# Kernel tuning notes

Hardware: AMD Instinct MI355X
Metric: run time of the kernel (lower is better)

## Reference

```python
import jax, jax.numpy as jnp
import numpy as np

N_NODES = 100000
N_EDGES = 1600000
IN_DIM = 128
HID = 64
HEADS = 8
OUTF = HID // HEADS  # out_feats per head = 8
ATTN_SLOPE = 0.2     # DGL GATConv leaky_relu slope for attention logits
ACT_SLOPE = 0.01     # F.leaky_relu default slope for inter-layer activation


def leaky_relu(x, slope):
    return jnp.where(x >= 0, x, slope * x)


def gat_layer(x, src, dst, W, al, ar, b, apply_act):
    # x: [N, Din], W: [Din, H*F], al/ar: [H, F], b: [H*F]
    N = x.shape[0]
    feat = (x @ W).reshape(N, HEADS, OUTF)                     # [N, H, F]
    el = jnp.sum(feat * al[None], axis=-1)                      # [N, H]
    er = jnp.sum(feat * ar[None], axis=-1)                      # [N, H]
    e = leaky_relu(el[src] + er[dst], ATTN_SLOPE)               # [E, H]
    # segment softmax over incoming edges of each dst node
    m = jax.ops.segment_max(e, dst, num_segments=N)             # [N, H]
    ex = jnp.exp(e - m[dst])                                    # [E, H]
    s = jax.ops.segment_sum(ex, dst, num_segments=N)            # [N, H]
    alpha = ex / s[dst]                                         # [E, H]
    msg = feat[src] * alpha[:, :, None]                         # [E, H, F]
    rst = jax.ops.segment_sum(msg, dst, num_segments=N)         # [N, H, F]
    rst = rst + b.reshape(1, HEADS, OUTF)
    if apply_act:
        rst = leaky_relu(rst, ACT_SLOPE)
    return rst.reshape(N, HEADS * OUTF)


def setup_inputs() -> dict:
    key = jax.random.key(0)
    ks = jax.random.split(key, 12)
    n_feat = jax.random.normal(ks[0], (N_NODES, IN_DIM), dtype=jnp.float32)
    src = jax.random.randint(ks[1], (N_EDGES,), 0, N_NODES, dtype=jnp.int32)
    dst = jax.random.randint(ks[2], (N_EDGES,), 0, N_NODES, dtype=jnp.int32)
    sc = 0.1
    W0 = sc * jax.random.normal(ks[3], (IN_DIM, HID), dtype=jnp.float32)
    al0 = sc * jax.random.normal(ks[4], (HEADS, OUTF), dtype=jnp.float32)
    ar0 = sc * jax.random.normal(ks[5], (HEADS, OUTF), dtype=jnp.float32)
    b0 = jnp.zeros((HID,), dtype=jnp.float32)
    W1 = sc * jax.random.normal(ks[6], (HID, HID), dtype=jnp.float32)
    al1 = sc * jax.random.normal(ks[7], (HEADS, OUTF), dtype=jnp.float32)
    ar1 = sc * jax.random.normal(ks[8], (HEADS, OUTF), dtype=jnp.float32)
    b1 = jnp.zeros((HID,), dtype=jnp.float32)
    return {"n_feat": n_feat, "src": src, "dst": dst,
            "W0": W0, "al0": al0, "ar0": ar0, "b0": b0,
            "W1": W1, "al1": al1, "ar1": ar1, "b1": b1}


def reference(n_feat, src, dst, W0, al0, ar0, b0, W1, al1, ar1, b1):
    h = gat_layer(n_feat, src, dst, W0, al0, ar0, b0, apply_act=True)
    h = gat_layer(h, src, dst, W1, al1, ar1, b1, apply_act=False)
    return h
```

## Files before the change

### kernel.cpp

```cpp
#include <hip/hip_runtime.h>
#include <math.h>

#define NN 100000
#define NE 1600000
#define ATTN_SLOPE 0.2f
#define ACT_SLOPE 0.01f

#define NBUK 512
#define BK 196
#define NBLK 1024
#define CHUNK ((NE + NBLK - 1) / NBLK)
#define CAP 5120

typedef __attribute__((ext_vector_type(8))) short bf16x8;
typedef __attribute__((ext_vector_type(4))) float f32x4;

__global__ void __launch_bounds__(256) count_kernel(const int* __restrict__ dst,
                                                    int* __restrict__ counts) {
    __shared__ int h[NBUK];
    const int blk = blockIdx.x;
    for (int i = threadIdx.x; i < NBUK; i += 256) h[i] = 0;
    __syncthreads();
    const int beg = blk * CHUNK;
    const int end = (beg + CHUNK < NE) ? beg + CHUNK : NE;
    for (int i = beg + threadIdx.x; i < end; i += 256)
        atomicAdd(&h[dst[i] / BK], 1);
    __syncthreads();
    for (int i = threadIdx.x; i < NBUK; i += 256)
        counts[blk * NBUK + i] = h[i];
}

__global__ void __launch_bounds__(NBLK) scanA(const int* __restrict__ counts,
                                              int* __restrict__ wbase, int* __restrict__ btot) {
    __shared__ int lds[NBLK];
    const int b = blockIdx.x;
    const int t = threadIdx.x;
    const int v = counts[t * NBUK + b];
    lds[t] = v;
    __syncthreads();
    for (int off = 1; off < NBLK; off <<= 1) {
        int u = (t >= off) ? lds[t - off] : 0;
        __syncthreads();
        lds[t] += u;
        __syncthreads();
    }
    wbase[t * NBUK + b] = lds[t] - v;
    if (t == NBLK - 1) btot[b] = lds[t];
}

__global__ void __launch_bounds__(NBUK) scan_bucket(const int* __restrict__ btot,
                                                    int* __restrict__ bbase, int* __restrict__ offs) {
    __shared__ int lds[NBUK];
    const int t = threadIdx.x;
    const int v = btot[t];
    lds[t] = v;
    __syncthreads();
    for (int off = 1; off < NBUK; off <<= 1) {
        int u = (t >= off) ? lds[t - off] : 0;
        __syncthreads();
        lds[t] += u;
        __syncthreads();
    }
    bbase[t] = lds[t] - v;
    if (t == NBUK - 1) { bbase[NBUK] = lds[t]; offs[NN] = lds[t]; }
}

__global__ void __launch_bounds__(256) scatter_radix(const int* __restrict__ src,
                                                     const int* __restrict__ dst,
                                                     const int* __restrict__ wbase,
                                                     const int* __restrict__ bbase,
                                                     int* __restrict__ tmp) {
    __shared__ int base[NBUK];
    __shared__ int cur[NBUK];
    const int blk = blockIdx.x;
    for (int i = threadIdx.x; i < NBUK; i += 256) {
        base[i] = bbase[i] + wbase[blk * NBUK + i];
        cur[i] = 0;
    }
    __syncthreads();
    const int beg = blk * CHUNK;
    const int end = (beg + CHUNK < NE) ? beg + CHUNK : NE;
    for (int i = beg + threadIdx.x; i < end; i += 256) {
        const int d = dst[i];
        const int b = d / BK;
        const int r = atomicAdd(&cur[b], 1);
        tmp[base[b] + r] = (src[i] << 8) | (d - b * BK);
    }
}

__global__ void __launch_bounds__(256) bucket_build(const int* __restrict__ tmp,
                                                    const int* __restrict__ bbase,
                                                    int* __restrict__ offs,
                                                    int* __restrict__ csr_src) {
    __shared__ int epack[CAP];
    __shared__ int csr_loc[CAP];
    __shared__ int cnt[256];
    __shared__ int loff[256];
    const int b = blockIdx.x;
    const int t = threadIdx.x;
    const int ebeg = bbase[b];
    const int nE = bbase[b + 1] - ebeg;
    const int nlo = b * BK;
    const int nn = (nlo < NN) ? ((NN - nlo < BK) ? (NN - nlo) : BK) : 0;
    const bool fits = (nE <= CAP);

    cnt[t] = 0;
    __syncthreads();
    for (int i = t; i < nE; i += 256) {
        const int p = tmp[ebeg + i];
        if (fits) epack[i] = p;
        atomicAdd(&cnt[p & 255], 1);
    }
    __syncthreads();
    const int v = cnt[t];
    for (int off = 1; off < 256; off <<= 1) {
        int u = (t >= off) ? cnt[t - off] : 0;
        __syncthreads();
        cnt[t] += u;
        __syncthreads();
    }
    const int excl = cnt[t] - v;
    loff[t] = excl;
    __syncthreads();
    cnt[t] = 0;
    if (t < nn) offs[nlo + t] = ebeg + excl;
    __syncthreads();
    for (int i = t; i < nE; i += 256) {
        const int p = fits ? epack[i] : tmp[ebeg + i];
        const int dloc = p & 255;
        const int pos = loff[dloc] + atomicAdd(&cnt[dloc], 1);
        if (fits) csr_loc[pos] = p >> 8;
        else csr_src[ebeg + pos] = p >> 8;
    }
    __syncthreads();
    if (fits)
        for (int i = t; i < nE; i += 256) csr_src[ebeg + i] = csr_loc[i];
}

__device__ __forceinline__ unsigned short bfr(float f) {
    unsigned int u = __builtin_bit_cast(unsigned int, f);
    return (unsigned short)((u + 0x7fffu + ((u >> 16) & 1u)) >> 16);
}
__device__ __forceinline__ float bf2f(unsigned short h) {
    return __builtin_bit_cast(float, ((unsigned int)h) << 16);
}
__device__ __forceinline__ float leaky_attn(float e) {
    return fmaf(0.4f, fabsf(e), 0.6f * e);
}

template <int DIN>
__global__ void __launch_bounds__(256) gemm_mfma_kernel(
        const float* __restrict__ x, const float* __restrict__ W,
        const float* __restrict__ al, const float* __restrict__ ar,
        unsigned short* __restrict__ feat, float* __restrict__ el, float* __restrict__ er,
        int nPairTiles) {
    constexpr int KS = DIN / 32;
    const int lane = threadIdx.x & 63;
    const int tw = threadIdx.x >> 6;
    const int colhalf = tw & 1;
    const int l15 = lane & 15;
    const int g = lane >> 4;
    const int colbase = colhalf * 32;

    bf16x8 Bhi[KS][2], Blo[KS][2];
#pragma unroll
    for (int ks = 0; ks < KS; ++ks) {
#pragma unroll
        for (int ct = 0; ct < 2; ++ct) {
            const int col = colbase + ct * 16 + l15;
#pragma unroll
            for (int j = 0; j < 8; ++j) {
                float w = W[(ks * 32 + g * 8 + j) * 64 + col];
                unsigned short h = bfr(w);
                Bhi[ks][ct][j] = (short)h;
                Blo[ks][ct][j] = (short)bfr(w - bf2f(h));
            }
        }
    }
    const float alc0 = al[colbase + l15];
    const float arc0 = ar[colbase + l15];
    const float alc1 = al[colbase + 16 + l15];
    const float arc1 = ar[colbase + 16 + l15];

#pragma unroll 1
    for (int pt = blockIdx.x; pt < nPairTiles; pt += gridDim.x) {
        const int rb = pt * 32 + (tw >> 1) * 16;
        f32x4 acc0 = {0.f, 0.f, 0.f, 0.f};
        f32x4 acc1 = {0.f, 0.f, 0.f, 0.f};
#pragma unroll
        for (int ks = 0; ks < KS; ++ks) {
            const float* xp = x + (size_t)(rb + l15) * DIN + ks * 32 + g * 8;
            f32x4 xa = *(const f32x4*)xp;
            f32x4 xb = *(const f32x4*)(xp + 4);
            bf16x8 Ahi, Alo;
#pragma unroll
            for (int j = 0; j < 4; ++j) {
                unsigned short h = bfr(xa[j]);
                Ahi[j] = (short)h;
                Alo[j] = (short)bfr(xa[j] - bf2f(h));
            }
#pragma unroll
            for (int j = 0; j < 4; ++j) {
                unsigned short h = bfr(xb[j]);
                Ahi[4 + j] = (short)h;
                Alo[4 + j] = (short)bfr(xb[j] - bf2f(h));
            }
            acc0 = __builtin_amdgcn_mfma_f32_16x16x32_bf16(Ahi, Bhi[ks][0], acc0, 0, 0, 0);
            acc0 = __builtin_amdgcn_mfma_f32_16x16x32_bf16(Ahi, Blo[ks][0], acc0, 0, 0, 0);
            acc0 = __builtin_amdgcn_mfma_f32_16x16x32_bf16(Alo, Bhi[ks][0], acc0, 0, 0, 0);
            acc1 = __builtin_amdgcn_mfma_f32_16x16x32_bf16(Ahi, Bhi[ks][1], acc1, 0, 0, 0);
            acc1 = __builtin_amdgcn_mfma_f32_16x16x32_bf16(Ahi, Blo[ks][1], acc1, 0, 0, 0);
            acc1 = __builtin_amdgcn_mfma_f32_16x16x32_bf16(Alo, Bhi[ks][1], acc1, 0, 0, 0);
        }
#pragma unroll
        for (int i = 0; i < 4; ++i) {
            const int n = rb + g * 4 + i;
            feat[(size_t)n * 64 + colbase + l15] = bfr(acc0[i]);
            feat[(size_t)n * 64 + colbase + 16 + l15] = bfr(acc1[i]);
            float vl0 = acc0[i] * alc0, vr0 = acc0[i] * arc0;
            float vl1 = acc1[i] * alc1, vr1 = acc1[i] * arc1;
#pragma unroll
            for (int d = 1; d < 8; d <<= 1) {
                vl0 += __shfl_xor(vl0, d); vr0 += __shfl_xor(vr0, d);
                vl1 += __shfl_xor(vl1, d); vr1 += __shfl_xor(vr1, d);
            }
            if ((lane & 7) == 0) {
                const int hb = (l15 >> 3) & 1;
                const int h0 = colbase / 8;
                el[n * 8 + h0 + hb] = vl0;
                er[n * 8 + h0 + hb] = vr0;
                el[n * 8 + h0 + 2 + hb] = vl1;
                er[n * 8 + h0 + 2 + hb] = vr1;
            }
        }
    }
}

__global__ void __launch_bounds__(128) aggregate_kernel(
        const unsigned short* __restrict__ feat, const float* __restrict__ el,
        const float* __restrict__ er,
        const int* __restrict__ csr_src, const int* __restrict__ offs,
        const float* __restrict__ bias, float* __restrict__ out, int N, int apply_act) {
    const int lane = threadIdx.x & 63;
    int node = (blockIdx.x << 1) + (threadIdx.x >> 6);
    if (node >= N) return;
    node = __builtin_amdgcn_readfirstlane(node);
    const int h = lane >> 3;
    const int beg = __builtin_amdgcn_readfirstlane(offs[node]);
    const int end = __builtin_amdgcn_readfirstlane(offs[node + 1]);
    const float er_n = er[node * 8 + h];

    float s0a = 0.f, s1a = 0.f, a0a = 0.f, a1a = 0.f;

    if (beg < end) {
        int si[8];
#pragma unroll
        for (int j = 0; j < 8; ++j) {
            const int idx = beg + j;
            si[j] = csr_src[idx < end ? idx : end - 1];
        }
#pragma unroll 1
        for (int k = beg; k < end; k += 8) {
            const int kn = k + 8;
            int sn[8];
            if (kn < end) {
#pragma unroll
                for (int j = 0; j < 8; ++j) {
                    const int idx = kn + j;
                    sn[j] = csr_src[idx < end ? idx : end - 1];
                }
            }
            unsigned short fu[8];
            float ev[8];
#pragma unroll
            for (int j = 0; j < 8; ++j) fu[j] = feat[(unsigned)(si[j] * 64 + lane)];
#pragma unroll
            for (int j = 0; j < 8; ++j) ev[j] = el[(unsigned)(si[j] * 8 + h)] + er_n;
#pragma unroll
            for (int j = 0; j < 8; ++j) {
                float p = __expf(leaky_attn(ev[j]));
                p = (k + j < end) ? p : 0.f;
                if (j & 1) { s1a += p; a1a = fmaf(p, bf2f(fu[j]), a1a); }
                else       { s0a += p; a0a = fmaf(p, bf2f(fu[j]), a0a); }
            }
            if (kn < end) {
#pragma unroll
                for (int j = 0; j < 8; ++j) si[j] = sn[j];
            }
        }
    }

    const float s = s0a + s1a;
    const float acc = a0a + a1a;
    float r = (s > 0.f) ? (acc / s) : 0.f;
    r += bias[lane];
    if (apply_act) r = (r >= 0.f) ? r : ACT_SLOPE * r;
    out[(size_t)node * 64 + lane] = r;
}

extern "C" void kernel_launch(void* const* d_in, const int* in_sizes, int n_in,
                              void* d_out, int out_size, void* d_ws, size_t ws_size,
                              hipStream_t stream) {
    const float* n_feat = (const float*)d_in[0];
    const int*   src    = (const int*)d_in[1];
    const int*   dst    = (const int*)d_in[2];
    const float* W0     = (const float*)d_in[3];
    const float* al0    = (const float*)d_in[4];
    const float* ar0    = (const float*)d_in[5];
    const float* b0     = (const float*)d_in[6];
    const float* W1     = (const float*)d_in[7];
    const float* al1    = (const float*)d_in[8];
    const float* ar1    = (const float*)d_in[9];
    const float* b1     = (const float*)d_in[10];
    float* out = (float*)d_out;

    char* ws = (char*)d_ws;
    size_t off = 0;
    auto alloc = [&](size_t bytes) -> void* {
        void* p = ws + off;
        off += (bytes + 255) & ~(size_t)255;
        return p;
    };
    unsigned short* featA = (unsigned short*)alloc((size_t)NN * 64 * 2);
    float* featB   = (float*)alloc((size_t)NN * 64 * 4);
    float* el      = (float*)alloc((size_t)NN * 8 * 4);
    float* er      = (float*)alloc((size_t)NN * 8 * 4);
    int*   offs    = (int*)alloc((size_t)(NN + 1) * 4);
    int*   csr_src = (int*)alloc((size_t)NE * 4);
    int*   tmp     = (int*)alloc((size_t)NE * 4);
    int*   counts  = (int*)alloc((size_t)NBLK * NBUK * 4);
    int*   wbase   = (int*)alloc((size_t)NBLK * NBUK * 4);
    int*   btot    = (int*)alloc((size_t)NBUK * 4);
    int*   bbase   = (int*)alloc((size_t)(NBUK + 1) * 4);

    count_kernel<<<NBLK, 256, 0, stream>>>(dst, counts);
    scanA<<<NBUK, NBLK, 0, stream>>>(counts, wbase, btot);
    scan_bucket<<<1, NBUK, 0, stream>>>(btot, bbase, offs);
    scatter_radix<<<NBLK, 256, 0, stream>>>(src, dst, wbase, bbase, tmp);
    bucket_build<<<NBUK, 256, 0, stream>>>(tmp, bbase, offs, csr_src);

    const int nPairTiles = NN / 32;

    gemm_mfma_kernel<128><<<nPairTiles, 256, 0, stream>>>(n_feat, W0, al0, ar0, featA, el, er, nPairTiles);
    aggregate_kernel<<<(NN + 1) / 2, 128, 0, stream>>>(featA, el, er, csr_src, offs, b0, featB, NN, 1);

    gemm_mfma_kernel<64><<<nPairTiles, 256, 0, stream>>>(featB, W1, al1, ar1, featA, el, er, nPairTiles);
    aggregate_kernel<<<(NN + 1) / 2, 128, 0, stream>>>(featA, el, er, csr_src, offs, b1, out, NN, 0);
}
```

Measured before the change: 211.7 us.

## Split wavefront into two half-waves processing alternate edges with packed bf16 loads

The aggregate kernel now lets each 32-lane half of the wavefront handle a different incoming edge, with each lane loading two packed bf16 features as one 32-bit word instead of one 16-bit value. The two halves are combined with a cross-half shuffle before one half writes a float2. This halves the exp and attention-logit work per lane and widens each memory access. In exchange it drops the software prefetch of the next batch of source indices and adds a tail loop plus a shuffle reduction.

```diff
diff --git a/kernel.cpp b/kernel.cpp
--- a/kernel.cpp
+++ b/kernel.cpp
@@ -245,57 +245,61 @@
     int node = (blockIdx.x << 1) + (threadIdx.x >> 6);
     if (node >= N) return;
     node = __builtin_amdgcn_readfirstlane(node);
-    const int h = lane >> 3;
+    const int e2 = lane >> 5;
+    const int l32 = lane & 31;
+    const int h = l32 >> 2;
     const int beg = __builtin_amdgcn_readfirstlane(offs[node]);
     const int end = __builtin_amdgcn_readfirstlane(offs[node + 1]);
     const float er_n = er[node * 8 + h];
 
-    float s0a = 0.f, s1a = 0.f, a0a = 0.f, a1a = 0.f;
-
-    if (beg < end) {
+    float s = 0.f, ax = 0.f, ay = 0.f;
+    int k = beg;
+    for (; k + 8 <= end; k += 8) {
         int si[8];
 #pragma unroll
-        for (int j = 0; j < 8; ++j) {
-            const int idx = beg + j;
-            si[j] = csr_src[idx < end ? idx : end - 1];
-        }
-#pragma unroll 1
-        for (int k = beg; k < end; k += 8) {
-            const int kn = k + 8;
-            int sn[8];
-            if (kn < end) {
-#pragma unroll
-                for (int j = 0; j < 8; ++j) {
-                    const int idx = kn + j;
-                    sn[j] = csr_src[idx < end ? idx : end - 1];
-                }
-            }
-            unsigned short fu[8];
-            float ev[8];
-#pragma unroll
-            for (int j = 0; j < 8; ++j) fu[j] = feat[(unsigned)(si[j] * 64 + lane)];
-#pragma unroll
-            for (int j = 0; j < 8; ++j) ev[j] = el[(unsigned)(si[j] * 8 + h)] + er_n;
-#pragma unroll
-            for (int j = 0; j < 8; ++j) {
-                float p = __expf(leaky_attn(ev[j]));
-                p = (k + j < end) ? p : 0.f;
-                if (j & 1) { s1a += p; a1a = fmaf(p, bf2f(fu[j]), a1a); }
-                else       { s0a += p; a0a = fmaf(p, bf2f(fu[j]), a0a); }
-            }
-            if (kn < end) {
-#pragma unroll
-                for (int j = 0; j < 8; ++j) si[j] = sn[j];
-            }
-        }
-    }
-
-    const float s = s0a + s1a;
-    const float acc = a0a + a1a;
-    float r = (s > 0.f) ? (acc / s) : 0.f;
-    r += bias[lane];
-    if (apply_act) r = (r >= 0.f) ? r : ACT_SLOPE * r;
-    out[(size_t)node * 64 + lane] = r;
+        for (int j = 0; j < 8; ++j) si[j] = csr_src[k + j];
+        unsigned fv[4];
+        float ev[4];
+#pragma unroll
+        for (int pp = 0; pp < 4; ++pp) {
+            const int sj = si[2 * pp + e2];
+            fv[pp] = *(const unsigned*)(feat + ((unsigned)sj * 64 + l32 * 2));
+            ev[pp] = el[(unsigned)(sj * 8 + h)] + er_n;
+        }
+#pragma unroll
+        for (int pp = 0; pp < 4; ++pp) {
+            const float p = __expf(leaky_attn(ev[pp]));
+            s += p;
+            ax = fmaf(p, bf2f((unsigned short)(fv[pp] & 0xffff)), ax);
+            ay = fmaf(p, bf2f((unsigned short)(fv[pp] >> 16)), ay);
+        }
+    }
+    for (; k < end; k += 2) {
+        const int idx = k + e2;
+        const int sj = csr_src[idx < end ? idx : end - 1];
+        const unsigned fv = *(const unsigned*)(feat + ((unsigned)sj * 64 + l32 * 2));
+        float p = __expf(leaky_attn(el[(unsigned)(sj * 8 + h)] + er_n));
+        p = (idx < end) ? p : 0.f;
+        s += p;
+        ax = fmaf(p, bf2f((unsigned short)(fv & 0xffff)), ax);
+        ay = fmaf(p, bf2f((unsigned short)(fv >> 16)), ay);
+    }
+
+    s  += __shfl_xor(s, 32, 64);
+    ax += __shfl_xor(ax, 32, 64);
+    ay += __shfl_xor(ay, 32, 64);
+
+    float rx = (s > 0.f) ? (ax / s) : 0.f;
+    float ry = (s > 0.f) ? (ay / s) : 0.f;
+    rx += bias[l32 * 2];
+    ry += bias[l32 * 2 + 1];
+    if (apply_act) {
+        rx = (rx >= 0.f) ? rx : ACT_SLOPE * rx;
+        ry = (ry >= 0.f) ? ry : ACT_SLOPE * ry;
+    }
+    if (e2 == 0) {
+        *(float2*)(out + (size_t)node * 64 + l32 * 2) = make_float2(rx, ry);
+    }
 }
 
 extern "C" void kernel_launch(void* const* d_in, const int* in_sizes, int n_in,
```

Measured after the change: 216.7 us. +2.4%, slower.
